# Performance work log

Hardware: AMD Instinct MI355X
Metric: run time of the kernel (lower is better)

Reference implementation:

```python
import jax, jax.numpy as jnp
import numpy as np

L = 2       # num_layers
D = 256     # d_model
DFF = 1024  # d_ffn
NH = 8      # n_heads
NP = 4      # n_points
CIN = 512   # in_channels
B = 8
HH = 64
WW = 64
EPS = 1e-5


def setup_inputs() -> dict:
    key = jax.random.key(0)
    ks = iter(jax.random.split(key, 48))
    def w(shape, s=0.02):
        return jax.random.normal(next(ks), shape, jnp.float32) * s
    inp = dict(
        x=jax.random.normal(next(ks), (B, CIN, HH, WW), jnp.float32),
        W_in=w((D, CIN)),
        bn1_g=jnp.ones((D,), jnp.float32), bn1_b=jnp.zeros((D,), jnp.float32),
        bn1_m=jnp.zeros((D,), jnp.float32), bn1_v=jnp.ones((D,), jnp.float32),
        query_embed=w((HH * WW, D), 1.0),
        Woff=w((L, D, NH * NP * 2)), boff=w((L, NH * NP * 2), 2.0),
        Wattn=w((L, D, NH * NP)), battn=jnp.zeros((L, NH * NP), jnp.float32),
        Wval=w((L, D, D)), bval=jnp.zeros((L, D), jnp.float32),
        Wo=w((L, D, D)), bo=jnp.zeros((L, D), jnp.float32),
        ln1_g=jnp.ones((L, D), jnp.float32), ln1_b=jnp.zeros((L, D), jnp.float32),
        W1=w((L, D, DFF)), b1=jnp.zeros((L, DFF), jnp.float32),
        W2=w((L, DFF, D)), b2=jnp.zeros((L, D), jnp.float32),
        ln2_g=jnp.ones((L, D), jnp.float32), ln2_b=jnp.zeros((L, D), jnp.float32),
        W_out=w((CIN, D)),
        bn2_g=jnp.ones((CIN,), jnp.float32), bn2_b=jnp.zeros((CIN,), jnp.float32),
        bn2_m=jnp.zeros((CIN,), jnp.float32), bn2_v=jnp.ones((CIN,), jnp.float32),
    )
    return inp


def layer_norm(x, g, b):
    m = jnp.mean(x, axis=-1, keepdims=True)
    v = jnp.mean((x - m) ** 2, axis=-1, keepdims=True)
    return (x - m) * jax.lax.rsqrt(v + EPS) * g + b


def bilinear_sample(value, loc, Hh, Ww):
    # value: (B, NH, dh, H*W); loc: (B, Lq, NH, NP, 2) normalized to [0,1]
    # Matches F.grid_sample(align_corners=False, padding_mode='zeros') with grid=2*loc-1.
    Bn, Lq, nH, P, _ = loc.shape
    gx = loc[..., 0] * Ww - 0.5
    gy = loc[..., 1] * Hh - 0.5
    x0 = jnp.floor(gx)
    y0 = jnp.floor(gy)
    wx = gx - x0
    wy = gy - y0
    x0i = x0.astype(jnp.int32)
    y0i = y0.astype(jnp.int32)

    def t(a):  # (B,Lq,NH,P) -> (B,NH,1,Lq*P)
        return jnp.transpose(a, (0, 2, 1, 3)).reshape(Bn, nH, 1, Lq * P)

    def gather(xi, yi):
        valid = (xi >= 0) & (xi < Ww) & (yi >= 0) & (yi < Hh)
        xc = jnp.clip(xi, 0, Ww - 1)
        yc = jnp.clip(yi, 0, Hh - 1)
        idx = t(yc * Ww + xc)  # (B,NH,1,Lq*P)
        v = jnp.take_along_axis(value, idx, axis=3)  # (B,NH,dh,Lq*P)
        return v * t(valid).astype(value.dtype)

    v00 = gather(x0i, y0i)
    v10 = gather(x0i + 1, y0i)
    v01 = gather(x0i, y0i + 1)
    v11 = gather(x0i + 1, y0i + 1)
    wxt = t(wx)
    wyt = t(wy)
    out = (v00 * (1 - wxt) * (1 - wyt) + v10 * wxt * (1 - wyt)
           + v01 * (1 - wxt) * wyt + v11 * wxt * wyt)
    return out.reshape(Bn, nH, -1, Lq, P)  # (B,NH,dh,Lq,NP)


def reference(x, W_in, bn1_g, bn1_b, bn1_m, bn1_v, query_embed,
              Woff, boff, Wattn, battn, Wval, bval, Wo, bo,
              ln1_g, ln1_b, W1, b1, W2, b2, ln2_g, ln2_b,
              W_out, bn2_g, bn2_b, bn2_m, bn2_v):
    Bn, C, Hh, Ww = x.shape
    HW = Hh * Ww
    dh = D // NH

    # proj_in: 1x1 conv (no bias) + BN (inference) + ReLU
    xp = jnp.einsum('bchw,dc->bdhw', x, W_in)
    xp = (xp - bn1_m[:, None, None]) * jax.lax.rsqrt(bn1_v[:, None, None] + EPS)
    xp = jax.nn.relu(xp * bn1_g[:, None, None] + bn1_b[:, None, None])
    src = xp.reshape(Bn, D, HW).transpose(0, 2, 1)  # (B, HW, D)

    # reference points: centers of pixels, normalized
    ry = (jnp.arange(Hh, dtype=jnp.float32) + 0.5) / Hh
    rx = (jnp.arange(Ww, dtype=jnp.float32) + 0.5) / Ww
    yy, xx = jnp.meshgrid(ry, rx, indexing='ij')
    refpts = jnp.stack([xx, yy], axis=-1).reshape(HW, 2)  # (HW, 2) as (x, y)
    norm = jnp.array([Ww, Hh], jnp.float32)

    q = jnp.broadcast_to(query_embed[None], (Bn, HW, D))
    for i in range(L):
        # --- MSDeformAttn (n_levels=1) ---
        val = (src @ Wval[i] + bval[i]).reshape(Bn, HW, NH, dh)
        val = val.transpose(0, 2, 3, 1)  # (B, NH, dh, HW)
        off = (q @ Woff[i] + boff[i]).reshape(Bn, HW, NH, NP, 2)
        attn = jax.nn.softmax((q @ Wattn[i] + battn[i]).reshape(Bn, HW, NH, NP), axis=-1)
        loc = refpts[None, :, None, None, :] + off / norm  # (B, HW, NH, NP, 2)
        samp = bilinear_sample(val, loc, Hh, Ww)  # (B, NH, dh, HW, NP)
        o = jnp.einsum('bhdqp,bhqp->bqhd', samp, attn.transpose(0, 2, 1, 3))
        o = o.reshape(Bn, HW, D) @ Wo[i] + bo[i]
        q = layer_norm(q + o, ln1_g[i], ln1_b[i])
        # --- FFN ---
        ffn = jax.nn.relu(q @ W1[i] + b1[i]) @ W2[i] + b2[i]
        q = layer_norm(q + ffn, ln2_g[i], ln2_b[i])

    # proj_out: 1x1 conv (no bias) + BN (inference) + ReLU
    y = q.transpose(0, 2, 1).reshape(Bn, D, Hh, Ww)
    y = jnp.einsum('bdhw,cd->bchw', y, W_out)
    y = (y - bn2_m[:, None, None]) * jax.lax.rsqrt(bn2_v[:, None, None] + EPS)
    return jax.nn.relu(y * bn2_g[:, None, None] + bn2_b[:, None, None])
```

## Files before the change

### kernel.cpp

```cpp
#include <hip/hip_runtime.h>
#include <cstdint>

#define LYR 2
#define DM  256
#define DFFN 1024
#define CINC 512
#define BBATCH 8
#define HWTOT 4096
#define EPSV 1e-5f

using u16 = unsigned short;
typedef __attribute__((ext_vector_type(8))) short bf16x8;
typedef __attribute__((ext_vector_type(4))) float f32x4;

__device__ inline u16 f2b(float v) {
    union { float f; uint32_t u; } x; x.f = v;
    uint32_t r = x.u + 0x7fffu + ((x.u >> 16) & 1u);
    return (u16)(r >> 16);
}
__device__ inline uint32_t pk2(float a, float b) {
    return (uint32_t)f2b(a) | ((uint32_t)f2b(b) << 16);
}
__device__ inline float blo(uint32_t d) {
    union { uint32_t i; float f; } x; x.i = d << 16; return x.f;
}
__device__ inline float bhi(uint32_t d) {
    union { uint32_t i; float f; } x; x.i = d & 0xffff0000u; return x.f;
}

template<int MODE>
__global__ __launch_bounds__(256) void mfma_gemm(
    const u16* __restrict__ A, const u16* __restrict__ Bt,
    const float* __restrict__ scale, const float* __restrict__ shift,
    void* __restrict__ Cv, int M, int N, int K, int ldc,
    long long a_zs, long long b_zs, long long c_zs, int swz, int gxlog)
{
    __shared__ u16 As[2][4096];
    __shared__ u16 Bs[2][4096];
    const int tid = threadIdx.x;
    const int lane = tid & 63;
    const int wid = tid >> 6;
    const int wm = (wid & 1) << 6, wn = (wid >> 1) << 6;
    const int quad = lane >> 4, r = lane & 15;

    int bx = blockIdx.x, by = blockIdx.y;
    if (swz) {
        int linear = by * gridDim.x + bx;
        int xcd = linear & 7;
        int s = linear >> 3;
        bx = s & (gridDim.x - 1);
        by = xcd * (gridDim.y >> 3) + (s >> gxlog);
    }
    const int m0 = by << 7, n0 = bx << 7;
    const u16* Ab = A + (long long)blockIdx.z * a_zs + (long long)m0 * K;
    const u16* Bb = Bt + (long long)blockIdx.z * b_zs + (long long)n0 * K;

    const int u0 = tid, u1 = tid + 256;
    const int mu0 = u0 >> 2, cu0 = (u0 & 3) ^ ((mu0 >> 1) & 3);
    const int mu1 = u1 >> 2, cu1 = (u1 & 3) ^ ((mu1 >> 1) & 3);
    const long long ga0 = (long long)mu0 * K + cu0 * 8;
    const long long ga1 = (long long)mu1 * K + cu1 * 8;

    int aoff[4], boff[4];
#pragma unroll
    for (int t = 0; t < 4; ++t) {
        int m = wm + t * 16 + r;
        aoff[t] = (m * 4 + (quad ^ ((m >> 1) & 3))) * 8;
        int n = wn + t * 16 + r;
        boff[t] = (n * 4 + (quad ^ ((n >> 1) & 3))) * 8;
    }

    f32x4 acc[4][4];
#pragma unroll
    for (int i = 0; i < 4; ++i)
#pragma unroll
        for (int j = 0; j < 4; ++j) acc[i][j] = (f32x4){0.f, 0.f, 0.f, 0.f};

    const int NT = K >> 5;
    __builtin_amdgcn_global_load_lds((const __attribute__((address_space(1))) void*)(Ab + ga0),
                                     (__attribute__((address_space(3))) void*)(&As[0][u0 * 8]), 16, 0, 0);
    __builtin_amdgcn_global_load_lds((const __attribute__((address_space(1))) void*)(Ab + ga1),
                                     (__attribute__((address_space(3))) void*)(&As[0][u1 * 8]), 16, 0, 0);
    __builtin_amdgcn_global_load_lds((const __attribute__((address_space(1))) void*)(Bb + ga0),
                                     (__attribute__((address_space(3))) void*)(&Bs[0][u0 * 8]), 16, 0, 0);
    __builtin_amdgcn_global_load_lds((const __attribute__((address_space(1))) void*)(Bb + ga1),
                                     (__attribute__((address_space(3))) void*)(&Bs[0][u1 * 8]), 16, 0, 0);
    __syncthreads();

    for (int t = 0; t < NT; ++t) {
        if (t + 1 < NT) {
            const int kn = (t + 1) << 5;
            const int nb = (t + 1) & 1;
            __builtin_amdgcn_global_load_lds((const __attribute__((address_space(1))) void*)(Ab + ga0 + kn),
                                             (__attribute__((address_space(3))) void*)(&As[nb][u0 * 8]), 16, 0, 0);
            __builtin_amdgcn_global_load_lds((const __attribute__((address_space(1))) void*)(Ab + ga1 + kn),
                                             (__attribute__((address_space(3))) void*)(&As[nb][u1 * 8]), 16, 0, 0);
            __builtin_amdgcn_global_load_lds((const __attribute__((address_space(1))) void*)(Bb + ga0 + kn),
                                             (__attribute__((address_space(3))) void*)(&Bs[nb][u0 * 8]), 16, 0, 0);
            __builtin_amdgcn_global_load_lds((const __attribute__((address_space(1))) void*)(Bb + ga1 + kn),
                                             (__attribute__((address_space(3))) void*)(&Bs[nb][u1 * 8]), 16, 0, 0);
        }
        const u16* Ap = As[t & 1];
        const u16* Bp = Bs[t & 1];
        bf16x8 af[4], bf[4];
#pragma unroll
        for (int tt = 0; tt < 4; ++tt) af[tt] = *(const bf16x8*)(Ap + aoff[tt]);
#pragma unroll
        for (int tt = 0; tt < 4; ++tt) bf[tt] = *(const bf16x8*)(Bp + boff[tt]);
#pragma unroll
        for (int i = 0; i < 4; ++i)
#pragma unroll
            for (int j = 0; j < 4; ++j)
                acc[i][j] = __builtin_amdgcn_mfma_f32_16x16x32_bf16(bf[j], af[i], acc[i][j], 0, 0, 0);
        __syncthreads();
    }

    const long long zc = (long long)blockIdx.z * c_zs;
    float4 sh4[4], sc4[4];
    if (MODE != 3) {
#pragma unroll
        for (int j = 0; j < 4; ++j) {
            int colb = n0 + wn + j * 16 + quad * 4;
            sh4[j] = *(const float4*)&shift[colb];
            if (MODE == 1) sc4[j] = *(const float4*)&scale[colb];
        }
    }
#pragma unroll
    for (int i = 0; i < 4; ++i) {
        const int row = m0 + wm + i * 16 + r;
        float rsc = 0.f, rsh = 0.f;
        if (MODE == 3) { rsc = scale[row]; rsh = shift[row]; }
#pragma unroll
        for (int j = 0; j < 4; ++j) {
            const int colb = n0 + wn + j * 16 + quad * 4;
            f32x4 v = acc[i][j];
            if (MODE == 0) {
                uint2 o;
                o.x = pk2(v[0] + sh4[j].x, v[1] + sh4[j].y);
                o.y = pk2(v[2] + sh4[j].z, v[3] + sh4[j].w);
                *(uint2*)((u16*)Cv + zc + (long long)row * ldc + colb) = o;
            } else if (MODE == 1) {
                uint2 o;
                o.x = pk2(fmaxf(v[0] * sc4[j].x + sh4[j].x, 0.f), fmaxf(v[1] * sc4[j].y + sh4[j].y, 0.f));
                o.y = pk2(fmaxf(v[2] * sc4[j].z + sh4[j].z, 0.f), fmaxf(v[3] * sc4[j].w + sh4[j].w, 0.f));
                *(uint2*)((u16*)Cv + zc + (long long)row * ldc + colb) = o;
            } else if (MODE == 2) {
                float4 o = {v[0] + sh4[j].x, v[1] + sh4[j].y, v[2] + sh4[j].z, v[3] + sh4[j].w};
                *(float4*)((float*)Cv + zc + (long long)row * ldc + colb) = o;
            } else {
                float4 o = {fmaxf(v[0] * rsc + rsh, 0.f), fmaxf(v[1] * rsc + rsh, 0.f),
                            fmaxf(v[2] * rsc + rsh, 0.f), fmaxf(v[3] * rsc + rsh, 0.f)};
                *(float4*)((float*)Cv + zc + (long long)row * ldc + colb) = o;
            }
        }
    }
}

__global__ __launch_bounds__(512, 4) void mfma_gemm_ln(
    const u16* __restrict__ A, const u16* __restrict__ Bf,
    const float* __restrict__ bias,
    float* __restrict__ q, u16* __restrict__ q16,
    const float* __restrict__ g, const float* __restrict__ beta, int K)
{
    __shared__ u16 As[2][2048];
    __shared__ float red_s[8][64], red_ss[8][64];
    const int tid = threadIdx.x;
    const int lane = tid & 63;
    const int w = tid >> 6;
    const int quad = lane >> 4, r = lane & 15;
    const int m0 = blockIdx.x << 6;
    const u16* Ab = A + (long long)m0 * K;

    const int mA = tid >> 2, cA = (tid & 3) ^ ((mA >> 1) & 3);
    const long long gaA = (long long)mA * K + cA * 8;
    const bool stager = tid < 256;

    int aoff[4];
#pragma unroll
    for (int t = 0; t < 4; ++t) {
        int m = t * 16 + r;
        aoff[t] = (m * 4 + (quad ^ ((m >> 1) & 3))) * 8;
    }

    const u16* Bw = Bf + ((size_t)(2 * w) * 64 + lane) * 8;

    f32x4 acc[4][2];
#pragma unroll
    for (int i = 0; i < 4; ++i)
#pragma unroll
        for (int j = 0; j < 2; ++j) acc[i][j] = (f32x4){0.f, 0.f, 0.f, 0.f};

    const int NT = K >> 5;

    if (stager)
        __builtin_amdgcn_global_load_lds((const __attribute__((address_space(1))) void*)(Ab + gaA),
                                         (__attribute__((address_space(3))) void*)(&As[0][tid * 8]), 16, 0, 0);
    bf16x8 bc0 = *(const bf16x8*)(Bw);
    bf16x8 bc1 = *(const bf16x8*)(Bw + 512);
    __syncthreads();

    for (int t = 0; t < NT; ++t) {
        const int tn = (t + 1 < NT) ? (t + 1) : t;
        if (stager)
            __builtin_amdgcn_global_load_lds((const __attribute__((address_space(1))) void*)(Ab + gaA + (long long)tn * 32),
                                             (__attribute__((address_space(3))) void*)(&As[(t + 1) & 1][tid * 8]), 16, 0, 0);
        const u16* Bn = Bw + (size_t)tn * 8192;
        bf16x8 bn0 = *(const bf16x8*)(Bn);
        bf16x8 bn1 = *(const bf16x8*)(Bn + 512);

        const u16* Ac = As[t & 1];
        bf16x8 af[4];
#pragma unroll
        for (int tt = 0; tt < 4; ++tt) af[tt] = *(const bf16x8*)(Ac + aoff[tt]);
#pragma unroll
        for (int i = 0; i < 4; ++i) {
            acc[i][0] = __builtin_amdgcn_mfma_f32_16x16x32_bf16(bc0, af[i], acc[i][0], 0, 0, 0);
            acc[i][1] = __builtin_amdgcn_mfma_f32_16x16x32_bf16(bc1, af[i], acc[i][1], 0, 0, 0);
        }
        __syncthreads();
        bc0 = bn0; bc1 = bn1;
    }

    float4 sh2[2];
#pragma unroll
    for (int j = 0; j < 2; ++j)
        sh2[j] = *(const float4*)&bias[w * 32 + j * 16 + quad * 4];

    float s_[4] = {0.f, 0.f, 0.f, 0.f}, ss_[4] = {0.f, 0.f, 0.f, 0.f};
#pragma unroll
    for (int i = 0; i < 4; ++i) {
        const int row = m0 + i * 16 + r;
#pragma unroll
        for (int j = 0; j < 2; ++j) {
            const int colb = w * 32 + j * 16 + quad * 4;
            float4 qo = *(const float4*)&q[(size_t)row * DM + colb];
            acc[i][j][0] += sh2[j].x + qo.x;
            acc[i][j][1] += sh2[j].y + qo.y;
            acc[i][j][2] += sh2[j].z + qo.z;
            acc[i][j][3] += sh2[j].w + qo.w;
#pragma unroll
            for (int e = 0; e < 4; ++e) {
                s_[i] += acc[i][j][e];
                ss_[i] += acc[i][j][e] * acc[i][j][e];
            }
        }
    }
#pragma unroll
    for (int i = 0; i < 4; ++i) {
        s_[i] += __shfl_xor(s_[i], 16);  ss_[i] += __shfl_xor(ss_[i], 16);
        s_[i] += __shfl_xor(s_[i], 32);  ss_[i] += __shfl_xor(ss_[i], 32);
    }
    if (quad == 0) {
#pragma unroll
        for (int i = 0; i < 4; ++i) {
            red_s[w][i * 16 + r] = s_[i];
            red_ss[w][i * 16 + r] = ss_[i];
        }
    }
    __syncthreads();

    float mean[4], rstd[4];
#pragma unroll
    for (int i = 0; i < 4; ++i) {
        float S = 0.f, SS = 0.f;
#pragma unroll
        for (int w2 = 0; w2 < 8; ++w2) { S += red_s[w2][i * 16 + r]; SS += red_ss[w2][i * 16 + r]; }
        mean[i] = S * (1.0f / 256.0f);
        rstd[i] = rsqrtf(SS * (1.0f / 256.0f) - mean[i] * mean[i] + EPSV);
    }

    float4 g4[2], bt4[2];
#pragma unroll
    for (int j = 0; j < 2; ++j) {
        int colb = w * 32 + j * 16 + quad * 4;
        g4[j] = *(const float4*)&g[colb];
        bt4[j] = *(const float4*)&beta[colb];
    }
#pragma unroll
    for (int i = 0; i < 4; ++i) {
        const int row = m0 + i * 16 + r;
#pragma unroll
        for (int j = 0; j < 2; ++j) {
            const int colb = w * 32 + j * 16 + quad * 4;
            float o0 = (acc[i][j][0] - mean[i]) * rstd[i] * g4[j].x + bt4[j].x;
            float o1 = (acc[i][j][1] - mean[i]) * rstd[i] * g4[j].y + bt4[j].y;
            float o2 = (acc[i][j][2] - mean[i]) * rstd[i] * g4[j].z + bt4[j].z;
            float o3 = (acc[i][j][3] - mean[i]) * rstd[i] * g4[j].w + bt4[j].w;
            *(float4*)&q[(size_t)row * DM + colb] = make_float4(o0, o1, o2, o3);
            *(uint2*)(q16 + (size_t)row * DM + colb) = make_uint2(pk2(o0, o1), pk2(o2, o3));
        }
    }
}

__global__ __launch_bounds__(512) void ffn_fused(
    const u16* __restrict__ q16in, const u16* __restrict__ w1F, const u16* __restrict__ w2F,
    const float* __restrict__ b1, const float* __restrict__ b2,
    float* __restrict__ q, u16* __restrict__ q16,
    const float* __restrict__ g, const float* __restrict__ beta)
{
    __shared__ u16 Aq[16384];
    __shared__ u16 hF[16384];
    __shared__ float red_s[8][64], red_ss[8][64];
    const int tid = threadIdx.x;
    const int lane = tid & 63;
    const int w = tid >> 6;
    const int quad = lane >> 4, r = lane & 15;
    const int m0 = blockIdx.x << 6;

    const u16* Ab = q16in + (long long)m0 * DM;
#pragma unroll
    for (int i = 0; i < 4; ++i) {
        int u = tid + i * 512;
        int ks = u >> 8, v = u & 255;
        int m = v >> 2, c = (v & 3) ^ ((m >> 1) & 3);
        __builtin_amdgcn_global_load_lds((const __attribute__((address_space(1))) void*)(Ab + (long long)m * DM + ks * 32 + c * 8),
                                         (__attribute__((address_space(3))) void*)(Aq + u * 8), 16, 0, 0);
    }

    int aoff[4];
#pragma unroll
    for (int t = 0; t < 4; ++t) {
        int m = t * 16 + r;
        aoff[t] = (m * 4 + (quad ^ ((m >> 1) & 3))) * 8;
    }

    f32x4 acc2[4][2];
#pragma unroll
    for (int i = 0; i < 4; ++i)
#pragma unroll
        for (int j = 0; j < 2; ++j) acc2[i][j] = (f32x4){0.f, 0.f, 0.f, 0.f};

    __syncthreads();

    for (int qq = 0; qq < 4; ++qq) {
        f32x4 acc1[4][2];
#pragma unroll
        for (int i = 0; i < 4; ++i)
#pragma unroll
            for (int j = 0; j < 2; ++j) acc1[i][j] = (f32x4){0.f, 0.f, 0.f, 0.f};
#pragma unroll
        for (int ks = 0; ks < 8; ++ks) {
            const u16* bp = w1F + ((size_t)(ks * 64 + qq * 16 + w * 2) * 64 + lane) * 8;
            bf16x8 bf0 = *(const bf16x8*)bp;
            bf16x8 bf1 = *(const bf16x8*)(bp + 512);
            bf16x8 af[4];
#pragma unroll
            for (int t = 0; t < 4; ++t) af[t] = *(const bf16x8*)(Aq + ks * 2048 + aoff[t]);
#pragma unroll
            for (int i = 0; i < 4; ++i) {
                acc1[i][0] = __builtin_amdgcn_mfma_f32_16x16x32_bf16(bf0, af[i], acc1[i][0], 0, 0, 0);
                acc1[i][1] = __builtin_amdgcn_mfma_f32_16x16x32_bf16(bf1, af[i], acc1[i][1], 0, 0, 0);
            }
        }
        __syncthreads();

#pragma unroll
        for (int j = 0; j < 2; ++j) {
            const int cb = qq * 256 + w * 32 + j * 16 + quad * 4;
            const float4 b14 = *(const float4*)&b1[cb];
            const int lane2 = r | (((j * 2 + (quad >> 1)) & 3) << 4);
            const int eo = (quad & 1) * 4;
#pragma unroll
            for (int i = 0; i < 4; ++i) {
                f32x4 v = acc1[i][j];
                uint2 o;
                o.x = pk2(fmaxf(v[0] + b14.x, 0.f), fmaxf(v[1] + b14.y, 0.f));
                o.y = pk2(fmaxf(v[2] + b14.z, 0.f), fmaxf(v[3] + b14.w, 0.f));
                *(uint2*)(hF + ((w * 4 + i) * 64 + lane2) * 8 + eo) = o;
            }
        }
        __syncthreads();

#pragma unroll
        for (int ks = 0; ks < 8; ++ks) {
            const u16* bp = w2F + ((size_t)((qq * 8 + ks) * 16 + w * 2) * 64 + lane) * 8;
            bf16x8 bf0 = *(const bf16x8*)bp;
            bf16x8 bf1 = *(const bf16x8*)(bp + 512);
            bf16x8 af[4];
#pragma unroll
            for (int t = 0; t < 4; ++t) af[t] = *(const bf16x8*)(hF + ((ks * 4 + t) * 64 + lane) * 8);
#pragma unroll
            for (int i = 0; i < 4; ++i) {
                acc2[i][0] = __builtin_amdgcn_mfma_f32_16x16x32_bf16(bf0, af[i], acc2[i][0], 0, 0, 0);
                acc2[i][1] = __builtin_amdgcn_mfma_f32_16x16x32_bf16(bf1, af[i], acc2[i][1], 0, 0, 0);
            }
        }
    }

    float4 sh2[2];
#pragma unroll
    for (int j = 0; j < 2; ++j)
        sh2[j] = *(const float4*)&b2[w * 32 + j * 16 + quad * 4];

    float s_[4] = {0.f, 0.f, 0.f, 0.f}, ss_[4] = {0.f, 0.f, 0.f, 0.f};
#pragma unroll
    for (int i = 0; i < 4; ++i) {
        const int row = m0 + i * 16 + r;
#pragma unroll
        for (int j = 0; j < 2; ++j) {
            const int colb = w * 32 + j * 16 + quad * 4;
            float4 qo = *(const float4*)&q[(size_t)row * DM + colb];
            acc2[i][j][0] += sh2[j].x + qo.x;
            acc2[i][j][1] += sh2[j].y + qo.y;
            acc2[i][j][2] += sh2[j].z + qo.z;
            acc2[i][j][3] += sh2[j].w + qo.w;
#pragma unroll
            for (int e = 0; e < 4; ++e) {
                s_[i] += acc2[i][j][e];
                ss_[i] += acc2[i][j][e] * acc2[i][j][e];
            }
        }
    }
#pragma unroll
    for (int i = 0; i < 4; ++i) {
        s_[i] += __shfl_xor(s_[i], 16);  ss_[i] += __shfl_xor(ss_[i], 16);
        s_[i] += __shfl_xor(s_[i], 32);  ss_[i] += __shfl_xor(ss_[i], 32);
    }
    if (quad == 0) {
#pragma unroll
        for (int i = 0; i < 4; ++i) {
            red_s[w][i * 16 + r] = s_[i];
            red_ss[w][i * 16 + r] = ss_[i];
        }
    }
    __syncthreads();

    float mean[4], rstd[4];
#pragma unroll
    for (int i = 0; i < 4; ++i) {
        float S = 0.f, SS = 0.f;
#pragma unroll
        for (int w2 = 0; w2 < 8; ++w2) { S += red_s[w2][i * 16 + r]; SS += red_ss[w2][i * 16 + r]; }
        mean[i] = S * (1.0f / 256.0f);
        rstd[i] = rsqrtf(SS * (1.0f / 256.0f) - mean[i] * mean[i] + EPSV);
    }

    float4 g4[2], bt4[2];
#pragma unroll
    for (int j = 0; j < 2; ++j) {
        int colb = w * 32 + j * 16 + quad * 4;
        g4[j] = *(const float4*)&g[colb];
        bt4[j] = *(const float4*)&beta[colb];
    }
#pragma unroll
    for (int i = 0; i < 4; ++i) {
        const int row = m0 + i * 16 + r;
#pragma unroll
        for (int j = 0; j < 2; ++j) {
            const int colb = w * 32 + j * 16 + quad * 4;
            float o0 = (acc2[i][j][0] - mean[i]) * rstd[i] * g4[j].x + bt4[j].x;
            float o1 = (acc2[i][j][1] - mean[i]) * rstd[i] * g4[j].y + bt4[j].y;
            float o2 = (acc2[i][j][2] - mean[i]) * rstd[i] * g4[j].z + bt4[j].z;
            float o3 = (acc2[i][j][3] - mean[i]) * rstd[i] * g4[j].w + bt4[j].w;
            *(float4*)&q[(size_t)row * DM + colb] = make_float4(o0, o1, o2, o3);
            *(uint2*)(q16 + (size_t)row * DM + colb) = make_uint2(pk2(o0, o1), pk2(o2, o3));
        }
    }
}

__device__ __attribute__((noinline)) void tconv(const float* src, u16* dst, int K, int N, int tk, int tn)
{
    __shared__ float t[32][33];
    const int tx = threadIdx.x & 31, ty = threadIdx.x >> 5;
#pragma unroll
    for (int i = 0; i < 4; ++i)
        t[ty + i * 8][tx] = src[(size_t)(tk * 32 + ty + i * 8) * N + tn * 32 + tx];
    __syncthreads();
#pragma unroll
    for (int i = 0; i < 4; ++i)
        dst[(size_t)(tn * 32 + ty + i * 8) * K + tk * 32 + tx] = f2b(t[tx][ty + i * 8]);
}

__device__ __attribute__((noinline)) void tconv_oa(const float* Woff, const float* Wattn, u16* dst, int tk, int tn)
{
    __shared__ float t[32][33];
    const int tx = threadIdx.x & 31, ty = threadIdx.x >> 5;
#pragma unroll
    for (int i = 0; i < 4; ++i) {
        int k = tk * 32 + ty + i * 8, n = tn * 32 + tx;
        float v = (n < 64) ? Woff[k * 64 + n] : ((n < 96) ? Wattn[k * 32 + n - 64] : 0.f);
        t[ty + i * 8][tx] = v;
    }
    __syncthreads();
#pragma unroll
    for (int i = 0; i < 4; ++i)
        dst[(size_t)(tn * 32 + ty + i * 8) * 256 + tk * 32 + tx] = f2b(t[tx][ty + i * 8]);
}

__device__ __attribute__((noinline)) void frag_prep(const float* W, u16* dst, int ks, int nc, int N)
{
    __shared__ float t[32][256];
    const int tid = threadIdx.x;
#pragma unroll
    for (int kk = 0; kk < 32; ++kk)
        t[kk][tid] = W[(size_t)(ks * 32 + kk) * N + nc * 256 + tid];
    __syncthreads();
    const int NT16 = N >> 4;
#pragma unroll
    for (int i = 0; i < 4; ++i) {
        int idx = tid + i * 256;
        int nt = idx >> 6, l = idx & 63;
        int n = nt * 16 + (l & 15);
        int kb = (l >> 4) * 8;
        u16 o[8];
#pragma unroll
        for (int e = 0; e < 8; ++e) o[e] = f2b(t[kb + e][n]);
        *(uint4*)(dst + ((size_t)(ks * NT16 + nc * 16 + nt) * 64 + l) * 8) = *(const uint4*)o;
    }
}

__global__ __launch_bounds__(256) void prep_weights(
    const float* __restrict__ Wval, const float* __restrict__ Wo,
    const float* __restrict__ W1, const float* __restrict__ W2,
    const float* __restrict__ Woff, const float* __restrict__ Wattn,
    const float* __restrict__ boff, const float* __restrict__ battn,
    const float* __restrict__ W_in, const float* __restrict__ W_out,
    const float* __restrict__ bn1g, const float* __restrict__ bn1b,
    const float* __restrict__ bn1m, const float* __restrict__ bn1v,
    const float* __restrict__ bn2g, const float* __restrict__ bn2b,
    const float* __restrict__ bn2m, const float* __restrict__ bn2v,
    u16* __restrict__ wvalT, u16* __restrict__ woF, u16* __restrict__ w1F,
    u16* __restrict__ w2F, u16* __restrict__ woaT,
    u16* __restrict__ winC, u16* __restrict__ woutC,
    float* __restrict__ bn1sc, float* __restrict__ bn1sh,
    float* __restrict__ bn2sc, float* __restrict__ bn2sh, float* __restrict__ boa)
{
    int bid = blockIdx.x;
    if (bid < 128) {
        int l = bid >> 6, r2 = bid & 63;
        tconv(Wval + l * 65536, wvalT + l * 65536, 256, 256, r2 & 7, r2 >> 3);
    } else if (bid < 192) {
        int i2 = bid - 128, l = i2 >> 5, r2 = i2 & 31;
        tconv_oa(Woff + l * 16384, Wattn + l * 8192, woaT + l * 32768, r2 & 7, r2 >> 3);
    } else if (bid < 208) {
        int i2 = bid - 192;
        frag_prep(Wo + (i2 >> 3) * 65536, woF + (i2 >> 3) * 65536, i2 & 7, 0, 256);
    } else if (bid < 272) {
        int i2 = bid - 208, l = i2 >> 5, r2 = i2 & 31;
        frag_prep(W1 + l * 262144, w1F + l * 262144, r2 >> 2, r2 & 3, 1024);
    } else if (bid < 336) {
        int i2 = bid - 272;
        frag_prep(W2 + (i2 >> 5) * 262144, w2F + (i2 >> 5) * 262144, i2 & 31, 0, 256);
    } else if (bid < 368) {
        int g2 = bid - 336, base = g2 * 4096, t = threadIdx.x;
#pragma unroll
        for (int k = 0; k < 16; ++k) winC[base + k * 256 + t] = f2b(W_in[base + k * 256 + t]);
    } else if (bid < 400) {
        int g2 = bid - 368, base = g2 * 4096, t = threadIdx.x;
#pragma unroll
        for (int k = 0; k < 16; ++k) woutC[base + k * 256 + t] = f2b(W_out[base + k * 256 + t]);
    } else {
        int t = threadIdx.x;
        { float s = bn1g[t] * rsqrtf(bn1v[t] + EPSV); bn1sc[t] = s; bn1sh[t] = bn1b[t] - bn1m[t] * s; }
        for (int c = 0; c < 2; ++c) {
            int i = c * 256 + t;
            float s = bn2g[i] * rsqrtf(bn2v[i] + EPSV);
            bn2sc[i] = s; bn2sh[i] = bn2b[i] - bn2m[i] * s;
        }
        if (t < 128)
            for (int l = 0; l < 2; ++l)
                boa[l * 128 + t] = (t < 64) ? boff[l * 64 + t]
                                 : ((t < 96) ? battn[l * 32 + t - 64] : 0.f);
    }
}

__global__ __launch_bounds__(256) void transpose_x(const float* __restrict__ x, u16* __restrict__ xT)
{
    __shared__ float t[64][65];
    const int b = blockIdx.z, p0 = blockIdx.y << 6, c0 = blockIdx.x << 6;
    const int tx = threadIdx.x & 63, ty = threadIdx.x >> 6;
    const float* xb = x + ((size_t)b * CINC + c0) * HWTOT + p0;
#pragma unroll
    for (int i = 0; i < 16; ++i)
        t[ty + i * 4][tx] = xb[(size_t)(ty + i * 4) * HWTOT + tx];
    __syncthreads();
    u16* xo = xT + ((size_t)b * HWTOT + p0) * CINC + c0;
#pragma unroll
    for (int i = 0; i < 16; ++i)
        xo[(size_t)(ty + i * 4) * CINC + tx] = f2b(t[tx][ty + i * 4]);
}

struct IW { int eo; float w; };

__global__ __launch_bounds__(256) void sample_kernel(
    const u16* __restrict__ val,
    const float* __restrict__ oa,
    u16* __restrict__ oms)
{
    __shared__ float s_oa[8][96];
    __shared__ IW s_iw[8][32][5];
    const int t = threadIdx.x;
    const int bq0 = blockIdx.x << 3;
    const int b = blockIdx.x >> 9;

    {
        int qi = t >> 5, j = t & 31;
        if (j < 24)
            ((float4*)s_oa[qi])[j] = ((const float4*)oa)[((size_t)(bq0 + qi)) * 32 + j];
    }
    __syncthreads();

    {
        const int qi = t >> 5, hp = t & 31, h = hp >> 2, p = hp & 3;
        const float* so = s_oa[qi];
        float l0 = so[64 + h * 4 + 0], l1 = so[64 + h * 4 + 1];
        float l2 = so[64 + h * 4 + 2], l3 = so[64 + h * 4 + 3];
        float mx = fmaxf(fmaxf(l0, l1), fmaxf(l2, l3));
        float e0 = __expf(l0 - mx), e1 = __expf(l1 - mx), e2 = __expf(l2 - mx), e3 = __expf(l3 - mx);
        float inv = 1.0f / (e0 + e1 + e2 + e3);
        float aw = ((p == 0) ? e0 : (p == 1) ? e1 : (p == 2) ? e2 : e3) * inv;
        const int bq = bq0 + qi;
        float gx = (float)(bq & 63) + so[hp * 2 + 0];
        float gy = (float)((bq >> 6) & 63) + so[hp * 2 + 1];
        float x0f = floorf(gx), y0f = floorf(gy);
        float wx = gx - x0f, wy = gy - y0f;
        int x0 = (int)x0f, y0 = (int)y0f;
#pragma unroll
        for (int c = 0; c < 4; ++c) {
            int xi = x0 + (c & 1), yi = y0 + (c >> 1);
            bool ok = (xi >= 0) && (xi < 64) && (yi >= 0) && (yi < 64);
            float wgt = ((c & 1) ? wx : 1.0f - wx) * ((c >> 1) ? wy : 1.0f - wy);
            s_iw[qi][hp][c].eo = ok ? ((yi * 64 + xi) << 8) : 0;
            s_iw[qi][hp][c].w = ok ? aw * wgt : 0.f;
        }
    }
    __syncthreads();

    {
        const int qi = t >> 5, l = t & 31, h = l >> 2, cc = l & 3;
        const u16* base = val + ((size_t)b << 20) + (h << 5) + (cc << 3);
        float a[8] = {0.f, 0.f, 0.f, 0.f, 0.f, 0.f, 0.f, 0.f};
#pragma unroll
        for (int p = 0; p < 4; ++p)
#pragma unroll
            for (int c = 0; c < 4; ++c) {
                IW iw = s_iw[qi][(h << 2) + p][c];
                uint4 v = *(const uint4*)(base + iw.eo);
                a[0] += iw.w * blo(v.x); a[1] += iw.w * bhi(v.x);
                a[2] += iw.w * blo(v.y); a[3] += iw.w * bhi(v.y);
                a[4] += iw.w * blo(v.z); a[5] += iw.w * bhi(v.z);
                a[6] += iw.w * blo(v.w); a[7] += iw.w * bhi(v.w);
            }
        uint4 o;
        o.x = (uint32_t)f2b(a[0]) | ((uint32_t)f2b(a[1]) << 16);
        o.y = (uint32_t)f2b(a[2]) | ((uint32_t)f2b(a[3]) << 16);
        o.z = (uint32_t)f2b(a[4]) | ((uint32_t)f2b(a[5]) << 16);
        o.w = (uint32_t)f2b(a[6]) | ((uint32_t)f2b(a[7]) << 16);
        *(uint4*)(oms + (size_t)(bq0 + qi) * 256 + (h << 5) + (cc << 3)) = o;
    }
}

__global__ __launch_bounds__(256) void bcast_q(
    const float4* __restrict__ qe, float4* __restrict__ q, u16* __restrict__ q16)
{
    const int i = blockIdx.x * 256 + threadIdx.x;
    float4 v = qe[i];
    uint2 pk = make_uint2(pk2(v.x, v.y), pk2(v.z, v.w));
#pragma unroll
    for (int b = 0; b < BBATCH; ++b) {
        q[(size_t)b * 262144 + i] = v;
        ((uint2*)q16)[(size_t)b * 262144 + i] = pk;
    }
}

extern "C" void kernel_launch(void* const* d_in, const int* in_sizes, int n_in,
                              void* d_out, int out_size, void* d_ws, size_t ws_size,
                              hipStream_t stream)
{
    (void)in_sizes; (void)n_in; (void)out_size; (void)ws_size;
    const float* x     = (const float*)d_in[0];
    const float* W_in  = (const float*)d_in[1];
    const float* bn1_g = (const float*)d_in[2];
    const float* bn1_b = (const float*)d_in[3];
    const float* bn1_m = (const float*)d_in[4];
    const float* bn1_v = (const float*)d_in[5];
    const float* qe    = (const float*)d_in[6];
    const float* Woff  = (const float*)d_in[7];
    const float* boff  = (const float*)d_in[8];
    const float* Wattn = (const float*)d_in[9];
    const float* battn = (const float*)d_in[10];
    const float* Wval  = (const float*)d_in[11];
    const float* bval  = (const float*)d_in[12];
    const float* Wo    = (const float*)d_in[13];
    const float* bo    = (const float*)d_in[14];
    const float* ln1_g = (const float*)d_in[15];
    const float* ln1_b = (const float*)d_in[16];
    const float* W1    = (const float*)d_in[17];
    const float* b1    = (const float*)d_in[18];
    const float* W2    = (const float*)d_in[19];
    const float* b2    = (const float*)d_in[20];
    const float* ln2_g = (const float*)d_in[21];
    const float* ln2_b = (const float*)d_in[22];
    const float* W_out = (const float*)d_in[23];
    const float* bn2_g = (const float*)d_in[24];
    const float* bn2_b = (const float*)d_in[25];
    const float* bn2_m = (const float*)d_in[26];
    const float* bn2_v = (const float*)d_in[27];
    float* out = (float*)d_out;

    char* w = (char*)d_ws;
    char* pool    = w;          w += 67108864;
    float* q      = (float*)w;  w += 33554432;
    u16*  q16     = (u16*)w;    w += 16777216;
    u16*  src16   = (u16*)w;    w += 16777216;
    u16*  wvalT   = (u16*)w;    w += 262144;
    u16*  woF     = (u16*)w;    w += 262144;
    u16*  w1F     = (u16*)w;    w += 1048576;
    u16*  w2F     = (u16*)w;    w += 1048576;
    u16*  woaT    = (u16*)w;    w += 131072;
    u16*  winC    = (u16*)w;    w += 262144;
    u16*  woutC   = (u16*)w;    w += 262144;
    float* bn1sc  = (float*)w;  w += 1024;
    float* bn1sh  = (float*)w;  w += 1024;
    float* bn2sc  = (float*)w;  w += 2048;
    float* bn2sh  = (float*)w;  w += 2048;
    float* boa    = (float*)w;  w += 1024;

    u16*  xT     = (u16*)pool;
    u16*  val16  = (u16*)pool;
    float* offat = (float*)(pool + 16777216);
    u16*  oms16  = (u16*)(pool + 33554432);

    prep_weights<<<dim3(401), 256, 0, stream>>>(
        Wval, Wo, W1, W2, Woff, Wattn, boff, battn, W_in, W_out,
        bn1_g, bn1_b, bn1_m, bn1_v, bn2_g, bn2_b, bn2_m, bn2_v,
        wvalT, woF, w1F, w2F, woaT, winC, woutC, bn1sc, bn1sh, bn2sc, bn2sh, boa);
    transpose_x<<<dim3(CINC / 64, HWTOT / 64, BBATCH), 256, 0, stream>>>(x, xT);
    bcast_q<<<dim3(1024), 256, 0, stream>>>((const float4*)qe, (float4*)q, q16);

    mfma_gemm<1><<<dim3(2, 256, 1), 256, 0, stream>>>(
        xT, winC, bn1sc, bn1sh, src16, 32768, 256, 512, 256, 0, 0, 0, 1, 1);

    for (int l = 0; l < LYR; ++l) {
        mfma_gemm<0><<<dim3(2, 256, 1), 256, 0, stream>>>(
            src16, wvalT + l * 65536, nullptr, bval + l * 256, val16,
            32768, 256, 256, 256, 0, 0, 0, 1, 1);
        mfma_gemm<2><<<dim3(1, 256, 1), 256, 0, stream>>>(
            q16, woaT + l * 32768, nullptr, boa + l * 128, offat,
            32768, 128, 256, 128, 0, 0, 0, 1, 0);
        sample_kernel<<<dim3(4096), 256, 0, stream>>>(val16, offat, oms16);
        mfma_gemm_ln<<<dim3(512), 512, 0, stream>>>(
            oms16, woF + l * 65536, bo + l * 256, q, q16,
            ln1_g + l * 256, ln1_b + l * 256, 256);
        ffn_fused<<<dim3(512), 512, 0, stream>>>(
            q16, w1F + l * 262144, w2F + l * 262144,
            b1 + l * 1024, b2 + l * 256, q, q16,
            ln2_g + l * 256, ln2_b + l * 256);
    }

    mfma_gemm<3><<<dim3(32, 4, BBATCH), 256, 0, stream>>>(
        woutC, q16, bn2sc, bn2sh, out, 512, 4096, 256, 4096,
        0, (long long)HWTOT * DM, (long long)CINC * HWTOT, 0, 0);
}
```

Before: 466.1 us.

## Deepen GEMM LDS pipelines with explicit vmcnt waits and MFMA priority hints

The main MFMA GEMM moves from a double-buffered LDS pipeline to a 4-stage ring, keeping three tiles in flight. It replaces __syncthreads with explicit s_waitcnt vmcnt plus a single s_barrier per iteration. The GEMM+LayerNorm kernel gets a 3-buffer ring with prefetch distance two under the same manual wait scheme. The FFN kernel raises wave priority around its MFMA loops. This is meant to hide global-load latency and cut barrier stalls, but LDS use doubles, which may lower occupancy, and the hand-written vmcnt counts must match the number of outstanding loads exactly.

After: 458.1 us. No clear change (-1.7%).

```diff
diff --git a/kernel.cpp b/kernel.cpp
--- a/kernel.cpp
+++ b/kernel.cpp
@@ -35,8 +35,8 @@
     void* __restrict__ Cv, int M, int N, int K, int ldc,
     long long a_zs, long long b_zs, long long c_zs, int swz, int gxlog)
 {
-    __shared__ u16 As[2][4096];
-    __shared__ u16 Bs[2][4096];
+    __shared__ u16 As[4][4096];
+    __shared__ u16 Bs[4][4096];
     const int tid = threadIdx.x;
     const int lane = tid & 63;
     const int wid = tid >> 6;
@@ -77,31 +77,32 @@
         for (int j = 0; j < 4; ++j) acc[i][j] = (f32x4){0.f, 0.f, 0.f, 0.f};
 
     const int NT = K >> 5;
-    __builtin_amdgcn_global_load_lds((const __attribute__((address_space(1))) void*)(Ab + ga0),
-                                     (__attribute__((address_space(3))) void*)(&As[0][u0 * 8]), 16, 0, 0);
-    __builtin_amdgcn_global_load_lds((const __attribute__((address_space(1))) void*)(Ab + ga1),
-                                     (__attribute__((address_space(3))) void*)(&As[0][u1 * 8]), 16, 0, 0);
-    __builtin_amdgcn_global_load_lds((const __attribute__((address_space(1))) void*)(Bb + ga0),
-                                     (__attribute__((address_space(3))) void*)(&Bs[0][u0 * 8]), 16, 0, 0);
-    __builtin_amdgcn_global_load_lds((const __attribute__((address_space(1))) void*)(Bb + ga1),
-                                     (__attribute__((address_space(3))) void*)(&Bs[0][u1 * 8]), 16, 0, 0);
-    __syncthreads();
+
+#define GSTAGE(g, b) do {                                                                       \
+    const long long kk = (long long)(g) << 5;                                                   \
+    __builtin_amdgcn_global_load_lds((const __attribute__((address_space(1))) void*)(Ab + ga0 + kk), \
+        (__attribute__((address_space(3))) void*)(&As[b][u0 * 8]), 16, 0, 0);                   \
+    __builtin_amdgcn_global_load_lds((const __attribute__((address_space(1))) void*)(Ab + ga1 + kk), \
+        (__attribute__((address_space(3))) void*)(&As[b][u1 * 8]), 16, 0, 0);                   \
+    __builtin_amdgcn_global_load_lds((const __attribute__((address_space(1))) void*)(Bb + ga0 + kk), \
+        (__attribute__((address_space(3))) void*)(&Bs[b][u0 * 8]), 16, 0, 0);                   \
+    __builtin_amdgcn_global_load_lds((const __attribute__((address_space(1))) void*)(Bb + ga1 + kk), \
+        (__attribute__((address_space(3))) void*)(&Bs[b][u1 * 8]), 16, 0, 0);                   \
+} while (0)
+
+    GSTAGE(0, 0);
+    GSTAGE(1, 1);
+    GSTAGE(2, 2);
 
     for (int t = 0; t < NT; ++t) {
-        if (t + 1 < NT) {
-            const int kn = (t + 1) << 5;
-            const int nb = (t + 1) & 1;
-            __builtin_amdgcn_global_load_lds((const __attribute__((address_space(1))) void*)(Ab + ga0 + kn),
-                                             (__attribute__((address_space(3))) void*)(&As[nb][u0 * 8]), 16, 0, 0);
-            __builtin_amdgcn_global_load_lds((const __attribute__((address_space(1))) void*)(Ab + ga1 + kn),
-                                             (__attribute__((address_space(3))) void*)(&As[nb][u1 * 8]), 16, 0, 0);
-            __builtin_amdgcn_global_load_lds((const __attribute__((address_space(1))) void*)(Bb + ga0 + kn),
-                                             (__attribute__((address_space(3))) void*)(&Bs[nb][u0 * 8]), 16, 0, 0);
-            __builtin_amdgcn_global_load_lds((const __attribute__((address_space(1))) void*)(Bb + ga1 + kn),
-                                             (__attribute__((address_space(3))) void*)(&Bs[nb][u1 * 8]), 16, 0, 0);
-        }
-        const u16* Ap = As[t & 1];
-        const u16* Bp = Bs[t & 1];
+        if (t < NT - 2)       asm volatile("s_waitcnt vmcnt(8)" ::: "memory");
+        else if (t == NT - 2) asm volatile("s_waitcnt vmcnt(4)" ::: "memory");
+        else                  asm volatile("s_waitcnt vmcnt(0)" ::: "memory");
+        __builtin_amdgcn_s_barrier();
+        __builtin_amdgcn_sched_barrier(0);
+        if (t + 3 < NT) GSTAGE(t + 3, (t + 3) & 3);
+        const u16* Ap = As[t & 3];
+        const u16* Bp = Bs[t & 3];
         bf16x8 af[4], bf[4];
 #pragma unroll
         for (int tt = 0; tt < 4; ++tt) af[tt] = *(const bf16x8*)(Ap + aoff[tt]);
@@ -112,8 +113,8 @@
 #pragma unroll
             for (int j = 0; j < 4; ++j)
                 acc[i][j] = __builtin_amdgcn_mfma_f32_16x16x32_bf16(bf[j], af[i], acc[i][j], 0, 0, 0);
-        __syncthreads();
-    }
+    }
+#undef GSTAGE
 
     const long long zc = (long long)blockIdx.z * c_zs;
     float4 sh4[4], sc4[4];
@@ -162,7 +163,7 @@
     float* __restrict__ q, u16* __restrict__ q16,
     const float* __restrict__ g, const float* __restrict__ beta, int K)
 {
-    __shared__ u16 As[2][2048];
+    __shared__ u16 As[3][2048];
     __shared__ float red_s[8][64], red_ss[8][64];
     const int tid = threadIdx.x;
     const int lane = tid & 63;
@@ -192,23 +193,33 @@
 
     const int NT = K >> 5;
 
-    if (stager)
+    if (stager) {
         __builtin_amdgcn_global_load_lds((const __attribute__((address_space(1))) void*)(Ab + gaA),
                                          (__attribute__((address_space(3))) void*)(&As[0][tid * 8]), 16, 0, 0);
+        __builtin_amdgcn_global_load_lds((const __attribute__((address_space(1))) void*)(Ab + gaA + 32),
+                                         (__attribute__((address_space(3))) void*)(&As[1][tid * 8]), 16, 0, 0);
+    }
+    __builtin_amdgcn_sched_barrier(0);
     bf16x8 bc0 = *(const bf16x8*)(Bw);
     bf16x8 bc1 = *(const bf16x8*)(Bw + 512);
-    __syncthreads();
-
+
+    int cb = 0;
     for (int t = 0; t < NT; ++t) {
-        const int tn = (t + 1 < NT) ? (t + 1) : t;
-        if (stager)
-            __builtin_amdgcn_global_load_lds((const __attribute__((address_space(1))) void*)(Ab + gaA + (long long)tn * 32),
-                                             (__attribute__((address_space(3))) void*)(&As[(t + 1) & 1][tid * 8]), 16, 0, 0);
-        const u16* Bn = Bw + (size_t)tn * 8192;
-        bf16x8 bn0 = *(const bf16x8*)(Bn);
-        bf16x8 bn1 = *(const bf16x8*)(Bn + 512);
-
-        const u16* Ac = As[t & 1];
+        asm volatile("s_waitcnt vmcnt(3)" ::: "memory");
+        __builtin_amdgcn_s_barrier();
+        __builtin_amdgcn_sched_barrier(0);
+        int nb = cb + 2; if (nb >= 3) nb -= 3;
+        if (stager && t + 2 < NT)
+            __builtin_amdgcn_global_load_lds((const __attribute__((address_space(1))) void*)(Ab + gaA + (long long)(t + 2) * 32),
+                                             (__attribute__((address_space(3))) void*)(&As[nb][tid * 8]), 16, 0, 0);
+        bf16x8 bn0, bn1;
+        if (t + 1 < NT) {
+            const u16* Bn = Bw + (size_t)(t + 1) * 8192;
+            bn0 = *(const bf16x8*)(Bn);
+            bn1 = *(const bf16x8*)(Bn + 512);
+        } else { bn0 = bc0; bn1 = bc1; }
+
+        const u16* Ac = As[cb];
         bf16x8 af[4];
 #pragma unroll
         for (int tt = 0; tt < 4; ++tt) af[tt] = *(const bf16x8*)(Ac + aoff[tt]);
@@ -217,8 +228,8 @@
             acc[i][0] = __builtin_amdgcn_mfma_f32_16x16x32_bf16(bc0, af[i], acc[i][0], 0, 0, 0);
             acc[i][1] = __builtin_amdgcn_mfma_f32_16x16x32_bf16(bc1, af[i], acc[i][1], 0, 0, 0);
         }
-        __syncthreads();
         bc0 = bn0; bc1 = bn1;
+        cb = (cb + 1 == 3) ? 0 : cb + 1;
     }
 
     float4 sh2[2];
@@ -338,6 +349,7 @@
         for (int i = 0; i < 4; ++i)
 #pragma unroll
             for (int j = 0; j < 2; ++j) acc1[i][j] = (f32x4){0.f, 0.f, 0.f, 0.f};
+        __builtin_amdgcn_s_setprio(1);
 #pragma unroll
         for (int ks = 0; ks < 8; ++ks) {
             const u16* bp = w1F + ((size_t)(ks * 64 + qq * 16 + w * 2) * 64 + lane) * 8;
@@ -352,6 +364,7 @@
                 acc1[i][1] = __builtin_amdgcn_mfma_f32_16x16x32_bf16(bf1, af[i], acc1[i][1], 0, 0, 0);
             }
         }
+        __builtin_amdgcn_s_setprio(0);
         __syncthreads();
 
 #pragma unroll
@@ -371,6 +384,7 @@
         }
         __syncthreads();
 
+        __builtin_amdgcn_s_setprio(1);
 #pragma unroll
         for (int ks = 0; ks < 8; ++ks) {
             const u16* bp = w2F + ((size_t)((qq * 8 + ks) * 16 + w * 2) * 64 + lane) * 8;
@@ -385,6 +399,7 @@
                 acc2[i][1] = __builtin_amdgcn_mfma_f32_16x16x32_bf16(bf1, af[i], acc2[i][1], 0, 0, 0);
             }
         }
+        __builtin_amdgcn_s_setprio(0);
     }
 
     float4 sh2[2];
```
